# Performance work log

Measured on AMD Instinct MI355X. Metric: run time of the kernel, lower is better.

## Reference

```python
import jax, jax.numpy as jnp
import numpy as np

IN_DIM = 128
OUT_DIM = 128
NUM_HEADS = 4
HEAD_DIM = OUT_DIM // NUM_HEADS  # 32
B, N = 4, 4096


def setup_inputs() -> dict:
    key = jax.random.key(0)
    ks = jax.random.split(key, 7)
    s_in = 1.0 / np.sqrt(IN_DIM)
    s_out = 1.0 / np.sqrt(OUT_DIM)
    return {
        "x": jax.random.normal(ks[0], (B, N, IN_DIM), dtype=jnp.float32),
        "adjacency": jax.random.randint(ks[1], (N, N), 0, 2, dtype=jnp.int32),
        "W_q": jax.random.uniform(ks[2], (IN_DIM, NUM_HEADS * HEAD_DIM), jnp.float32, -s_in, s_in),
        "W_k": jax.random.uniform(ks[3], (IN_DIM, NUM_HEADS * HEAD_DIM), jnp.float32, -s_in, s_in),
        "W_v": jax.random.uniform(ks[4], (IN_DIM, NUM_HEADS * HEAD_DIM), jnp.float32, -s_in, s_in),
        "W_o": jax.random.uniform(ks[5], (OUT_DIM, OUT_DIM), jnp.float32, -s_out, s_out),
        "b_o": jax.random.uniform(ks[6], (OUT_DIM,), jnp.float32, -s_out, s_out),
    }


def reference(x, adjacency, W_q, W_k, W_v, W_o, b_o):
    Bn, Nn, _ = x.shape
    # QKV projections -> (B, H, N, Dh)
    q = (x @ W_q).reshape(Bn, Nn, NUM_HEADS, HEAD_DIM).transpose(0, 2, 1, 3)
    k = (x @ W_k).reshape(Bn, Nn, NUM_HEADS, HEAD_DIM).transpose(0, 2, 1, 3)
    v = (x @ W_v).reshape(Bn, Nn, NUM_HEADS, HEAD_DIM).transpose(0, 2, 1, 3)
    scores = jnp.einsum("bhnd,bhmd->bhnm", q, k) / np.sqrt(HEAD_DIM).astype(np.float32)
    # adjacency mask (1,1,N,N): -inf where no edge
    adj = adjacency[None, None, :, :]
    scores = jnp.where(adj == 0, -jnp.inf, scores)
    attn = jax.nn.softmax(scores, axis=-1)
    out = jnp.einsum("bhnm,bhmd->bhnd", attn, v)
    out = out.transpose(0, 2, 1, 3).reshape(Bn, Nn, NUM_HEADS * HEAD_DIM)  # concat heads
    return out @ W_o + b_o
```

## Files before the change

kernel.cpp:

```cpp
#include <hip/hip_runtime.h>
#include <stdint.h>

typedef __attribute__((ext_vector_type(4))) short short4v;
typedef __attribute__((ext_vector_type(8))) short bf16x8;
typedef __attribute__((ext_vector_type(4))) float f32x4;
typedef __attribute__((ext_vector_type(2))) uint32_t uint2v;
typedef __attribute__((ext_vector_type(4))) uint32_t uint4v;
typedef __attribute__((ext_vector_type(4))) uint16_t ushort4v;

#define NN 4096

__device__ __forceinline__ uint16_t f2bf(float f) {
    union { float f; uint32_t u; } c; c.f = f;
    uint32_t r = c.u + 0x7FFF + ((c.u >> 16) & 1);
    return (uint16_t)(r >> 16);
}

__global__ __launch_bounds__(256) void pack_kernel(
    const int* __restrict__ adj, uint64_t* __restrict__ bits,
    const float* __restrict__ Wq, const float* __restrict__ Wk,
    const float* __restrict__ Wv, const float* __restrict__ Wo,
    uint16_t* __restrict__ WT, uint16_t* __restrict__ WoT)
{
    const int lane = threadIdx.x & 63;
    const int wave = (blockIdx.x * blockDim.x + threadIdx.x) >> 6;
    const int nwaves = (gridDim.x * blockDim.x) >> 6;
    const int TOT = (NN * NN) / 64;
    for (int i = wave; i < TOT; i += nwaves) {
        int v = adj[(size_t)i * 64 + lane];
        uint64_t m = __ballot(v != 0);
        if (lane == 0) bits[i] = m;
    }
    const int tid = blockIdx.x * blockDim.x + threadIdx.x;
    const int nth = gridDim.x * blockDim.x;
    for (int t = tid; t < 3 * 128 * 128 + 128 * 128; t += nth) {
        if (t < 3 * 128 * 128) {
            int j = t >> 7, k = t & 127;
            int m = j >> 7, jj = j & 127;
            const float* W = (m == 0) ? Wq : ((m == 1) ? Wk : Wv);
            float v = W[k * 128 + jj];
            if (m == 0) v *= (0.17677669529663687f * 1.4426950408889634f);
            WT[t] = f2bf(v);
        } else {
            int t2 = t - 3 * 128 * 128;
            int j = t2 >> 7, k = t2 & 127;
            WoT[t2] = f2bf(Wo[k * 128 + j]);
        }
    }
}

__global__ __launch_bounds__(256) void qkv_kernel(
    const float* __restrict__ x, const uint16_t* __restrict__ WT,
    uint16_t* __restrict__ Q, uint16_t* __restrict__ Kf, uint16_t* __restrict__ Vf)
{
    const int wave = threadIdx.x >> 6, lane = threadIdx.x & 63;
    const int g = lane >> 4, l15 = lane & 15;
    const int ntile = blockIdx.x * 4 + wave;
    const int n = ntile * 16 + l15;
    const int b = n >> 12, nn = n & 4095;

    const char* xrow = (const char*)x + (size_t)n * 512;
    bf16x8 xb[4];
#pragma unroll
    for (int ks = 0; ks < 4; ++ks) {
        f32x4 a = *(const f32x4*)(xrow + ks * 128 + g * 16);
        f32x4 c = *(const f32x4*)(xrow + ks * 128 + 64 + g * 16);
        bf16x8 f;
#pragma unroll
        for (int i = 0; i < 4; ++i) { f[i] = (short)f2bf(a[i]); f[4 + i] = (short)f2bf(c[i]); }
        xb[ks] = f;
    }

#pragma unroll 1
    for (int jt = 0; jt < 24; ++jt) {
        const int j0 = jt * 16;
        const char* wrow = (const char*)WT + (size_t)(j0 + l15) * 256;
        f32x4 acc = {0.f, 0.f, 0.f, 0.f};
#pragma unroll
        for (int ks = 0; ks < 4; ++ks) {
            short4v a0 = *(const short4v*)(wrow + ks * 64 + g * 8);
            short4v a1 = *(const short4v*)(wrow + ks * 64 + 32 + g * 8);
            bf16x8 af = __builtin_shufflevector(a0, a1, 0, 1, 2, 3, 4, 5, 6, 7);
            acc = __builtin_amdgcn_mfma_f32_16x16x32_bf16(af, xb[ks], acc, 0, 0, 0);
        }
        const int m = j0 >> 7;
        const int bh = b * 4 + ((j0 & 127) >> 5);
        if (m == 0) {
            const int d0 = (j0 & 31) + g * 4;
            ushort4v st;
#pragma unroll
            for (int r = 0; r < 4; ++r) st[r] = f2bf(acc[r]);
            *(ushort4v*)(Q + ((size_t)bh * 4096 + nn) * 32 + d0) = st;
        } else if (m == 1) {
            const int half = (j0 >> 4) & 1;
            ushort4v st;
#pragma unroll
            for (int r = 0; r < 4; ++r) st[r] = f2bf(acc[r]);
            *(ushort4v*)(Kf + ((size_t)bh << 17) + (ntile & 255) * 512 + lane * 8 + half * 4) = st;
        } else {
            const int half = (j0 >> 4) & 1;
            uint16_t* vb2 = Vf + ((size_t)bh << 17) + ((ntile & 255) >> 1) * 1024 + half * 512
                          + ((l15 >> 2) * 16 + g * 4) * 8 + (l15 & 3) + ((ntile & 1) << 2);
#pragma unroll
            for (int r = 0; r < 4; ++r) vb2[r * 8] = f2bf(acc[r]);
        }
    }
}

__global__ __launch_bounds__(256) void attn_kernel(
    const uint16_t* __restrict__ Q, const uint16_t* __restrict__ Kf,
    const uint16_t* __restrict__ Vf, const uint32_t* __restrict__ bits,
    uint16_t* __restrict__ O)
{
    __shared__ f32x4 cmb[4][4][2][64];
    __shared__ float csum[4][4][64];
    const int tid = threadIdx.x;
    const int wave = tid >> 6, lane = tid & 63;
    const int g = lane >> 4, l15 = lane & 15, gsh = g * 4;
    const int blk = blockIdx.x;
    const int bh = ((blk & 7) << 1) | ((blk >> 3) & 1);
    const int qb = blk >> 4;
    const int q0 = qb * 64;

    const char* Kp = (const char*)Kf + ((size_t)bh << 18) + wave * 65536 + lane * 16;
    const char* Vp = (const char*)Vf + ((size_t)bh << 18) + wave * 65536 + lane * 16;
    const uint32_t* ap[4];
#pragma unroll
    for (int qg = 0; qg < 4; ++qg)
        ap[qg] = bits + (size_t)(q0 + qg * 16 + l15) * 128 + wave * 32;

    bf16x8 qf[4];
#pragma unroll
    for (int qg = 0; qg < 4; ++qg) {
        const char* qrow = (const char*)Q + ((size_t)bh * 4096 + q0 + qg * 16 + l15) * 64;
        short4v a0 = *(const short4v*)(qrow + g * 8);
        short4v a1 = *(const short4v*)(qrow + 32 + g * 8);
        qf[qg] = __builtin_shufflevector(a0, a1, 0, 1, 2, 3, 4, 5, 6, 7);
    }

    bf16x8 ones;
#pragma unroll
    for (int i = 0; i < 8; ++i) ones[i] = (short)0x3F80;

    const f32x4 z = {0.f, 0.f, 0.f, 0.f};
    f32x4 o[4][2], sacc[4];
#pragma unroll
    for (int qg = 0; qg < 4; ++qg) { o[qg][0] = z; o[qg][1] = z; sacc[qg] = z; }

    bf16x8 kc[4], kn[4];
    uint2v wc[4], wn[4];
#pragma unroll
    for (int j = 0; j < 4; ++j) kc[j] = *(const bf16x8*)(Kp + j * 1024);
    Kp += 4096;
#pragma unroll
    for (int qg = 0; qg < 4; ++qg) { wc[qg] = *(const uint2v*)ap[qg]; ap[qg] += 2; }

    auto body = [&](bf16x8 (&kcur)[4], uint2v (&wcur)[4],
                    bf16x8 (&knxt)[4], uint2v (&wnxt)[4]) {
#pragma unroll
        for (int j = 0; j < 4; ++j) knxt[j] = *(const bf16x8*)(Kp + j * 1024);
        Kp += 4096;
#pragma unroll
        for (int qg = 0; qg < 4; ++qg) { wnxt[qg] = *(const uint2v*)ap[qg]; ap[qg] += 2; }
        bf16x8 vc[4];
#pragma unroll
        for (int i = 0; i < 4; ++i) vc[i] = *(const bf16x8*)(Vp + i * 1024);
        Vp += 4096;

#pragma unroll
        for (int qg = 0; qg < 4; ++qg) {
            f32x4 s[4];
#pragma unroll
            for (int j = 0; j < 4; ++j)
                s[j] = __builtin_amdgcn_mfma_f32_16x16x32_bf16(kcur[j], qf[qg], z, 0, 0, 0);
            float p[16];
#pragma unroll
            for (int j = 0; j < 4; ++j) {
                uint32_t wj = wcur[qg][j >> 1] >> (((j & 1) << 4) + gsh);
#pragma unroll
                for (int r = 0; r < 4; ++r) {
                    float pv = __builtin_amdgcn_exp2f(s[j][r]);
                    int msk = ((int)(wj << (31 - r))) >> 31;
                    p[j * 4 + r] = __uint_as_float(__float_as_uint(pv) & (uint32_t)msk);
                }
            }
            uint32_t pk[8];
#pragma unroll
            for (int i = 0; i < 8; ++i) {
                uint32_t r_;
                asm("v_cvt_pk_bf16_f32 %0, %1, %2" : "=v"(r_) : "v"(p[2 * i]), "v"(p[2 * i + 1]));
                pk[i] = r_;
            }
            uint4v u0 = {pk[0], pk[1], pk[2], pk[3]};
            uint4v u1 = {pk[4], pk[5], pk[6], pk[7]};
            bf16x8 pf0 = __builtin_bit_cast(bf16x8, u0);
            bf16x8 pf1 = __builtin_bit_cast(bf16x8, u1);
            o[qg][0] = __builtin_amdgcn_mfma_f32_16x16x32_bf16(vc[0], pf0, o[qg][0], 0, 0, 0);
            o[qg][0] = __builtin_amdgcn_mfma_f32_16x16x32_bf16(vc[2], pf1, o[qg][0], 0, 0, 0);
            o[qg][1] = __builtin_amdgcn_mfma_f32_16x16x32_bf16(vc[1], pf0, o[qg][1], 0, 0, 0);
            o[qg][1] = __builtin_amdgcn_mfma_f32_16x16x32_bf16(vc[3], pf1, o[qg][1], 0, 0, 0);
            sacc[qg] = __builtin_amdgcn_mfma_f32_16x16x32_bf16(ones, pf0, sacc[qg], 0, 0, 0);
            sacc[qg] = __builtin_amdgcn_mfma_f32_16x16x32_bf16(ones, pf1, sacc[qg], 0, 0, 0);
        }
    };

#pragma unroll 1
    for (int tt = 0; tt < 16; tt += 2) {
        body(kc, wc, kn, wn);
        body(kn, wn, kc, wc);
    }

#pragma unroll
    for (int qg = 0; qg < 4; ++qg) {
        cmb[wave][qg][0][lane] = o[qg][0];
        cmb[wave][qg][1][lane] = o[qg][1];
        csum[wave][qg][lane] = sacc[qg][0];
    }
    __syncthreads();
    {
        const int qg = wave;
        f32x4 a0 = cmb[0][qg][0][lane];
        f32x4 a1 = cmb[0][qg][1][lane];
        float sd = csum[0][qg][lane];
#pragma unroll
        for (int v = 1; v < 4; ++v) {
            a0 += cmb[v][qg][0][lane];
            a1 += cmb[v][qg][1][lane];
            sd += csum[v][qg][lane];
        }
        const float inv = 1.0f / sd;
        const int q = q0 + qg * 16 + l15;
        uint16_t* orow = O + ((size_t)bh * 4096 + q) * 32;
        ushort4v st0, st1;
#pragma unroll
        for (int r = 0; r < 4; ++r) {
            st0[r] = f2bf(a0[r] * inv);
            st1[r] = f2bf(a1[r] * inv);
        }
        *(ushort4v*)(orow + gsh) = st0;
        *(ushort4v*)(orow + 16 + gsh) = st1;
    }
}

__global__ __launch_bounds__(256) void proj_kernel(
    const uint16_t* __restrict__ A, const uint16_t* __restrict__ WoT,
    const float* __restrict__ bo, float* __restrict__ out)
{
    const int wave = threadIdx.x >> 6, lane = threadIdx.x & 63;
    const int g = lane >> 4, l15 = lane & 15;
    const int ntile = blockIdx.x * 4 + wave;
    const int n = ntile * 16 + l15;
    const int b = n >> 12, nn = n & 4095;

    bf16x8 bfr[4];
#pragma unroll
    for (int h = 0; h < 4; ++h) {
        const char* arow = (const char*)A + (((size_t)(b * 4 + h)) * 4096 + nn) * 64;
        short4v a0 = *(const short4v*)(arow + g * 8);
        short4v a1 = *(const short4v*)(arow + 32 + g * 8);
        bfr[h] = __builtin_shufflevector(a0, a1, 0, 1, 2, 3, 4, 5, 6, 7);
    }
#pragma unroll 1
    for (int ct = 0; ct < 8; ++ct) {
        const int c0 = ct * 16;
        const char* wrow = (const char*)WoT + (size_t)(c0 + l15) * 256;
        f32x4 acc = {0.f, 0.f, 0.f, 0.f};
#pragma unroll
        for (int h = 0; h < 4; ++h) {
            short4v a0 = *(const short4v*)(wrow + h * 64 + g * 8);
            short4v a1 = *(const short4v*)(wrow + h * 64 + 32 + g * 8);
            bf16x8 af = __builtin_shufflevector(a0, a1, 0, 1, 2, 3, 4, 5, 6, 7);
            acc = __builtin_amdgcn_mfma_f32_16x16x32_bf16(af, bfr[h], acc, 0, 0, 0);
        }
        f32x4 bias = *(const f32x4*)(bo + c0 + g * 4);
#pragma unroll
        for (int r = 0; r < 4; ++r) acc[r] += bias[r];
        *(f32x4*)(out + (size_t)n * 128 + c0 + g * 4) = acc;
    }
}

extern "C" void kernel_launch(void* const* d_in, const int* in_sizes, int n_in,
                              void* d_out, int out_size, void* d_ws, size_t ws_size,
                              hipStream_t stream)
{
    const float* x   = (const float*)d_in[0];
    const int*   adj = (const int*)d_in[1];
    const float* Wq  = (const float*)d_in[2];
    const float* Wk  = (const float*)d_in[3];
    const float* Wv  = (const float*)d_in[4];
    const float* Wo  = (const float*)d_in[5];
    const float* bo  = (const float*)d_in[6];
    float* out = (float*)d_out;

    char* ws = (char*)d_ws;
    uint16_t* Q    = (uint16_t*)(ws);
    uint16_t* Kf   = (uint16_t*)(ws + ((size_t)4 << 20));
    uint16_t* Vf   = (uint16_t*)(ws + ((size_t)8 << 20));
    uint16_t* AO   = (uint16_t*)(ws + ((size_t)12 << 20));
    uint32_t* bits = (uint32_t*)(ws + ((size_t)16 << 20));
    uint16_t* WT   = (uint16_t*)(ws + ((size_t)18 << 20));
    uint16_t* WoT  = (uint16_t*)(ws + ((size_t)18 << 20) + 98304);

    hipLaunchKernelGGL(pack_kernel, dim3(2048), dim3(256), 0, stream,
                       adj, (uint64_t*)bits, Wq, Wk, Wv, Wo, WT, WoT);
    hipLaunchKernelGGL(qkv_kernel, dim3(256), dim3(256), 0, stream,
                       x, WT, Q, Kf, Vf);
    hipLaunchKernelGGL(attn_kernel, dim3(1024), dim3(256), 0, stream,
                       Q, Kf, Vf, bits, AO);
    hipLaunchKernelGGL(proj_kernel, dim3(256), dim3(256), 0, stream,
                       AO, WoT, bo, out);
}
```

Measured before the change: 125.9 us.

## Split attention key range across eight waves and vectorize V stores

```diff
diff --git a/kernel.cpp b/kernel.cpp
--- a/kernel.cpp
+++ b/kernel.cpp
@@ -74,6 +74,7 @@
 #pragma unroll 1
     for (int jt = 0; jt < 24; ++jt) {
         const int j0 = jt * 16;
+        const bool isV = (j0 >= 256);
         const char* wrow = (const char*)WT + (size_t)(j0 + l15) * 256;
         f32x4 acc = {0.f, 0.f, 0.f, 0.f};
 #pragma unroll
@@ -81,33 +82,28 @@
             short4v a0 = *(const short4v*)(wrow + ks * 64 + g * 8);
             short4v a1 = *(const short4v*)(wrow + ks * 64 + 32 + g * 8);
             bf16x8 af = __builtin_shufflevector(a0, a1, 0, 1, 2, 3, 4, 5, 6, 7);
-            acc = __builtin_amdgcn_mfma_f32_16x16x32_bf16(af, xb[ks], acc, 0, 0, 0);
+            acc = isV ? __builtin_amdgcn_mfma_f32_16x16x32_bf16(xb[ks], af, acc, 0, 0, 0)
+                      : __builtin_amdgcn_mfma_f32_16x16x32_bf16(af, xb[ks], acc, 0, 0, 0);
         }
         const int m = j0 >> 7;
         const int bh = b * 4 + ((j0 & 127) >> 5);
+        const int half = (j0 >> 4) & 1;
+        ushort4v st;
+#pragma unroll
+        for (int r = 0; r < 4; ++r) st[r] = f2bf(acc[r]);
         if (m == 0) {
             const int d0 = (j0 & 31) + g * 4;
-            ushort4v st;
-#pragma unroll
-            for (int r = 0; r < 4; ++r) st[r] = f2bf(acc[r]);
             *(ushort4v*)(Q + ((size_t)bh * 4096 + nn) * 32 + d0) = st;
         } else if (m == 1) {
-            const int half = (j0 >> 4) & 1;
-            ushort4v st;
-#pragma unroll
-            for (int r = 0; r < 4; ++r) st[r] = f2bf(acc[r]);
             *(ushort4v*)(Kf + ((size_t)bh << 17) + (ntile & 255) * 512 + lane * 8 + half * 4) = st;
         } else {
-            const int half = (j0 >> 4) & 1;
-            uint16_t* vb2 = Vf + ((size_t)bh << 17) + ((ntile & 255) >> 1) * 1024 + half * 512
-                          + ((l15 >> 2) * 16 + g * 4) * 8 + (l15 & 3) + ((ntile & 1) << 2);
-#pragma unroll
-            for (int r = 0; r < 4; ++r) vb2[r * 8] = f2bf(acc[r]);
-        }
-    }
-}
-
-__global__ __launch_bounds__(256) void attn_kernel(
+            *(ushort4v*)(Vf + ((size_t)bh << 17) + ((ntile & 255) >> 1) * 1024
+                         + half * 512 + lane * 8 + ((ntile & 1) << 2)) = st;
+        }
+    }
+}
+
+__global__ __launch_bounds__(512, 5) void attn_kernel(
     const uint16_t* __restrict__ Q, const uint16_t* __restrict__ Kf,
     const uint16_t* __restrict__ Vf, const uint32_t* __restrict__ bits,
     uint16_t* __restrict__ O)
@@ -122,12 +118,12 @@
     const int qb = blk >> 4;
     const int q0 = qb * 64;
 
-    const char* Kp = (const char*)Kf + ((size_t)bh << 18) + wave * 65536 + lane * 16;
-    const char* Vp = (const char*)Vf + ((size_t)bh << 18) + wave * 65536 + lane * 16;
+    const char* Kp = (const char*)Kf + ((size_t)bh << 18) + wave * 32768 + lane * 16;
+    const char* Vp = (const char*)Vf + ((size_t)bh << 18) + wave * 32768 + lane * 16;
     const uint32_t* ap[4];
 #pragma unroll
     for (int qg = 0; qg < 4; ++qg)
-        ap[qg] = bits + (size_t)(q0 + qg * 16 + l15) * 128 + wave * 32;
+        ap[qg] = bits + (size_t)(q0 + qg * 16 + l15) * 128 + wave * 16;
 
     bf16x8 qf[4];
 #pragma unroll
@@ -147,36 +143,28 @@
 #pragma unroll
     for (int qg = 0; qg < 4; ++qg) { o[qg][0] = z; o[qg][1] = z; sacc[qg] = z; }
 
-    bf16x8 kc[4], kn[4];
-    uint2v wc[4], wn[4];
-#pragma unroll
-    for (int j = 0; j < 4; ++j) kc[j] = *(const bf16x8*)(Kp + j * 1024);
-    Kp += 4096;
-#pragma unroll
-    for (int qg = 0; qg < 4; ++qg) { wc[qg] = *(const uint2v*)ap[qg]; ap[qg] += 2; }
-
-    auto body = [&](bf16x8 (&kcur)[4], uint2v (&wcur)[4],
-                    bf16x8 (&knxt)[4], uint2v (&wnxt)[4]) {
-#pragma unroll
-        for (int j = 0; j < 4; ++j) knxt[j] = *(const bf16x8*)(Kp + j * 1024);
-        Kp += 4096;
-#pragma unroll
-        for (int qg = 0; qg < 4; ++qg) { wnxt[qg] = *(const uint2v*)ap[qg]; ap[qg] += 2; }
-        bf16x8 vc[4];
+#pragma unroll 1
+    for (int t = 0; t < 8; ++t) {
+        bf16x8 kc[4], vc[4];
+#pragma unroll
+        for (int j = 0; j < 4; ++j) kc[j] = *(const bf16x8*)(Kp + j * 1024);
 #pragma unroll
         for (int i = 0; i < 4; ++i) vc[i] = *(const bf16x8*)(Vp + i * 1024);
-        Vp += 4096;
+        Kp += 4096; Vp += 4096;
+        uint2v wc[4];
+#pragma unroll
+        for (int qg = 0; qg < 4; ++qg) { wc[qg] = *(const uint2v*)ap[qg]; ap[qg] += 2; }
 
 #pragma unroll
         for (int qg = 0; qg < 4; ++qg) {
             f32x4 s[4];
 #pragma unroll
             for (int j = 0; j < 4; ++j)
-                s[j] = __builtin_amdgcn_mfma_f32_16x16x32_bf16(kcur[j], qf[qg], z, 0, 0, 0);
+                s[j] = __builtin_amdgcn_mfma_f32_16x16x32_bf16(kc[j], qf[qg], z, 0, 0, 0);
             float p[16];
 #pragma unroll
             for (int j = 0; j < 4; ++j) {
-                uint32_t wj = wcur[qg][j >> 1] >> (((j & 1) << 4) + gsh);
+                uint32_t wj = wc[qg][j >> 1] >> (((j & 1) << 4) + gsh);
 #pragma unroll
                 for (int r = 0; r < 4; ++r) {
                     float pv = __builtin_amdgcn_exp2f(s[j][r]);
@@ -202,43 +190,40 @@
             sacc[qg] = __builtin_amdgcn_mfma_f32_16x16x32_bf16(ones, pf0, sacc[qg], 0, 0, 0);
             sacc[qg] = __builtin_amdgcn_mfma_f32_16x16x32_bf16(ones, pf1, sacc[qg], 0, 0, 0);
         }
-    };
-
-#pragma unroll 1
-    for (int tt = 0; tt < 16; tt += 2) {
-        body(kc, wc, kn, wn);
-        body(kn, wn, kc, wc);
-    }
-
-#pragma unroll
-    for (int qg = 0; qg < 4; ++qg) {
-        cmb[wave][qg][0][lane] = o[qg][0];
-        cmb[wave][qg][1][lane] = o[qg][1];
-        csum[wave][qg][lane] = sacc[qg][0];
+    }
+
+    if (wave < 4) {
+#pragma unroll
+        for (int qg = 0; qg < 4; ++qg) {
+            cmb[wave][qg][0][lane] = o[qg][0];
+            cmb[wave][qg][1][lane] = o[qg][1];
+            csum[wave][qg][lane] = sacc[qg][0];
+        }
+    }
+    __syncthreads();
+    if (wave >= 4) {
+        const int w2 = wave - 4;
+#pragma unroll
+        for (int qg = 0; qg < 4; ++qg) {
+            cmb[w2][qg][0][lane] += o[qg][0];
+            cmb[w2][qg][1][lane] += o[qg][1];
+            csum[w2][qg][lane] += sacc[qg][0];
+        }
     }
     __syncthreads();
     {
-        const int qg = wave;
-        f32x4 a0 = cmb[0][qg][0][lane];
-        f32x4 a1 = cmb[0][qg][1][lane];
-        float sd = csum[0][qg][lane];
-#pragma unroll
-        for (int v = 1; v < 4; ++v) {
-            a0 += cmb[v][qg][0][lane];
-            a1 += cmb[v][qg][1][lane];
-            sd += csum[v][qg][lane];
-        }
+        const int qg = wave & 3, h = wave >> 2;
+        f32x4 a = cmb[0][qg][h][lane] + cmb[1][qg][h][lane]
+                + cmb[2][qg][h][lane] + cmb[3][qg][h][lane];
+        float sd = csum[0][qg][lane] + csum[1][qg][lane]
+                 + csum[2][qg][lane] + csum[3][qg][lane];
         const float inv = 1.0f / sd;
         const int q = q0 + qg * 16 + l15;
         uint16_t* orow = O + ((size_t)bh * 4096 + q) * 32;
-        ushort4v st0, st1;
-#pragma unroll
-        for (int r = 0; r < 4; ++r) {
-            st0[r] = f2bf(a0[r] * inv);
-            st1[r] = f2bf(a1[r] * inv);
-        }
-        *(ushort4v*)(orow + gsh) = st0;
-        *(ushort4v*)(orow + 16 + gsh) = st1;
+        ushort4v st;
+#pragma unroll
+        for (int r = 0; r < 4; ++r) st[r] = f2bf(a[r] * inv);
+        *(ushort4v*)(orow + h * 16 + gsh) = st;
     }
 }
 
@@ -305,7 +290,7 @@
                        adj, (uint64_t*)bits, Wq, Wk, Wv, Wo, WT, WoT);
     hipLaunchKernelGGL(qkv_kernel, dim3(256), dim3(256), 0, stream,
                        x, WT, Q, Kf, Vf);
-    hipLaunchKernelGGL(attn_kernel, dim3(1024), dim3(256), 0, stream,
+    hipLaunchKernelGGL(attn_kernel, dim3(1024), dim3(512), 0, stream,
                        Q, Kf, Vf, bits, AO);
     hipLaunchKernelGGL(proj_kernel, dim3(256), dim3(256), 0, stream,
                        AO, WoT, bo, out);
```

Result: slower. 238.2 us (+89.3%).
